# Optimization experiments

Hardware: AMD Instinct MI355X
Metric: run time of the kernel (lower is better)

Reference implementation:

```python
import jax, jax.numpy as jnp
import numpy as np

N_NODES = 50000


def gcn_conv(x, W, b, src, dst, n_nodes):
    # PyG GCNConv: add self-loops, symmetric normalization, linear, scatter-add.
    loop = jnp.arange(n_nodes, dtype=src.dtype)
    s = jnp.concatenate([src, loop])  # [E+N]
    d = jnp.concatenate([dst, loop])
    deg = jax.ops.segment_sum(jnp.ones_like(d, dtype=x.dtype), d, num_segments=n_nodes)
    dinv = jnp.where(deg > 0, deg ** -0.5, 0.0)
    norm = dinv[s] * dinv[d]  # [E+N]
    h = x @ W  # [N, F_out] transform first (cheaper than per-edge)
    msg = h[s] * norm[:, None]  # gather + scale
    out = jax.ops.segment_sum(msg, d, num_segments=n_nodes)  # scatter-add
    return out + b


def setup_inputs() -> dict:
    key = jax.random.key(0)
    k1, k2, k3, k4, k5 = jax.random.split(key, 5)
    n_in, n_hid, n_out = 128, 128, 64
    x = jax.random.normal(k1, (N_NODES, n_in), dtype=jnp.float32)
    edge_index = jax.random.randint(k2, (2, 800000), 0, N_NODES, dtype=jnp.int64)
    edge_label_index = jax.random.randint(k3, (2, 200000), 0, N_NODES, dtype=jnp.int64)
    # Glorot-style init for GCN weights, zero bias (PyG default)
    W1 = jax.random.normal(k4, (n_in, n_hid), dtype=jnp.float32) * (1.0 / np.sqrt(n_in))
    W2 = jax.random.normal(k5, (n_hid, n_out), dtype=jnp.float32) * (1.0 / np.sqrt(n_hid))
    b1 = jnp.zeros((n_hid,), dtype=jnp.float32)
    b2 = jnp.zeros((n_out,), dtype=jnp.float32)
    return {"x": x, "edge_index": edge_index, "edge_label_index": edge_label_index,
            "W1": W1, "b1": b1, "W2": W2, "b2": b2}


def reference(x, edge_index, edge_label_index, W1, b1, W2, b2):
    src, dst = edge_index[0], edge_index[1]
    h = jax.nn.relu(gcn_conv(x, W1, b1, src, dst, N_NODES))
    z = gcn_conv(h, W2, b2, src, dst, N_NODES)
    # decode: per-edge dot product of endpoint embeddings
    logits = jnp.sum(z[edge_label_index[0]] * z[edge_label_index[1]], axis=-1)
    return logits
```

## Files before the change

kernel.cpp:

```cpp
#include <hip/hip_runtime.h>

#define N_NODES 50000
#define NB ((N_NODES + 255) / 256)

using half8 = __attribute__((ext_vector_type(8))) _Float16;
using half4 = __attribute__((ext_vector_type(4))) _Float16;
using f32x4 = __attribute__((ext_vector_type(4))) float;


#define OFF_ROWPTR 50048
#define OFF_DESC   100096
#define OFF_CNT    100608
#define OFF_ESRC   150656
#define OFF_EPOS   950656
#define OFF_W1T    1750656
#define OFF_W2T    1758848
#define OFF_H1B    1762944
#define OFF_OUT1   4962944
#define OFF_Z      8162944

__device__ __forceinline__ ushort f2bf(float f) {
  uint u = __float_as_uint(f);
  u += 0x7fffu + ((u >> 16) & 1u);
  return (ushort)(u >> 16);
}
__device__ __forceinline__ uint pack2(float a, float b) {
  return (uint)f2bf(a) | ((uint)f2bf(b) << 16);
}
__device__ __forceinline__ uint pack2h(float a, float b) {
  ushort ua = __builtin_bit_cast(ushort, (_Float16)a);
  ushort ub = __builtin_bit_cast(ushort, (_Float16)b);
  return (uint)ua | ((uint)ub << 16);
}
__device__ __forceinline__ float blo(uint u) { return __uint_as_float(u << 16); }
__device__ __forceinline__ float bhi(uint u) { return __uint_as_float(u & 0xffff0000u); }

__global__ __launch_bounds__(256) void k_zero_prep(int* __restrict__ cnt,
                                                   uint* __restrict__ desc,
                                                   const float* __restrict__ W1,
                                                   const float* __restrict__ W2,
                                                   _Float16* __restrict__ W1t,
                                                   _Float16* __restrict__ W2t) {
  int bid = blockIdx.x;
  if (bid < NB) {
    int i = bid * 256 + threadIdx.x;
    if (i < N_NODES) cnt[i] = 0;
    if (bid == 0 && threadIdx.x < NB) desc[threadIdx.x] = 0;
    return;
  }
  int i = (bid - NB) * 256 + threadIdx.x;
  if (i < 16384) {
    int c = i >> 7, k = i & 127;
    W1t[c * 128 + (k ^ ((c & 7) << 3))] = (_Float16)W1[k * 128 + c];
  } else if (i < 24576) {
    int j = i - 16384;
    int c = j >> 7, k = j & 127;
    W2t[c * 128 + (k ^ ((c & 7) << 3))] = (_Float16)W2[k * 64 + c];
  }
}

__global__ __launch_bounds__(256) void k_hist(const int* __restrict__ dst, int E,
                                              int* __restrict__ cnt,
                                              int* __restrict__ epos) {
  int i = blockIdx.x * 256 + threadIdx.x;
  if (i < E) epos[i] = atomicAdd(&cnt[dst[i]], 1);
}

__global__ __launch_bounds__(256) void k_scanlb(const int* __restrict__ cnt,
                                                int* __restrict__ rowptr,
                                                float* __restrict__ dinv,
                                                uint* __restrict__ desc, int E) {
  __shared__ int tmp[256];
  __shared__ int s_prefix;
  const int b = blockIdx.x;
  const int i = b * 256 + threadIdx.x;
  int v = (i < N_NODES) ? cnt[i] : 0;
  tmp[threadIdx.x] = v;
  __syncthreads();
  for (int off = 1; off < 256; off <<= 1) {
    int t = (threadIdx.x >= off) ? tmp[threadIdx.x - off] : 0;
    __syncthreads();
    tmp[threadIdx.x] += t;
    __syncthreads();
  }
  int incl = tmp[threadIdx.x];
  int total = tmp[255];

  if (threadIdx.x == 0) {
    uint w0 = (b == 0) ? ((2u << 30) | (uint)total) : ((1u << 30) | (uint)total);
    atomicExch(&desc[b], w0);
    if (b == 0) s_prefix = 0;
  }
  if (b > 0 && threadIdx.x < 64) {
    const int lane = threadIdx.x;
    int run = 0;
    int j = b - 1;
    while (true) {
      int jj = j - lane;
      uint w = (jj >= 0) ? atomicAdd(&desc[jj], 0u) : (2u << 30);
      uint st = w >> 30;
      unsigned long long mz = __ballot(st == 0u);
      unsigned long long mp = __ballot(st == 2u);
      int fp = mp ? (__ffsll((long long)mp) - 1) : 64;
      unsigned long long below = (fp >= 64) ? ~0ull : ((1ull << fp) - 1ull);
      if (mz & below) continue;
      int contrib = (lane <= fp) ? (int)(w & 0x3FFFFFFFu) : 0;
      contrib += __shfl_down(contrib, 32, 64);
      contrib += __shfl_down(contrib, 16, 64);
      contrib += __shfl_down(contrib, 8, 64);
      contrib += __shfl_down(contrib, 4, 64);
      contrib += __shfl_down(contrib, 2, 64);
      contrib += __shfl_down(contrib, 1, 64);
      run += __shfl(contrib, 0, 64);
      if (fp < 64) break;
      j -= 64;
    }
    if (lane == 0) {
      atomicExch(&desc[b], (2u << 30) | (uint)(run + total));
      s_prefix = run;
    }
  }
  __syncthreads();
  int run = s_prefix;
  if (i < N_NODES) {
    rowptr[i] = run + incl - v;
    dinv[i] = rsqrtf(1.0f + (float)v);
  }
  if (b == NB - 1 && threadIdx.x == 0) rowptr[N_NODES] = E;
}

__global__ __launch_bounds__(256) void k_fill(const int* __restrict__ src,
                                              const int* __restrict__ dst,
                                              const int* __restrict__ epos, int E,
                                              const int* __restrict__ rowptr,
                                              int* __restrict__ esrc) {
  int e = blockIdx.x * 256 + threadIdx.x;
  if (e < E) esrc[rowptr[dst[e]] + epos[e]] = src[e];
}

__global__ __launch_bounds__(256) void k_gemm1(const float* __restrict__ x,
                                               const _Float16* __restrict__ W1t,
                                               const float* __restrict__ dinv,
                                               ushort* __restrict__ h1b) {
  __shared__ _Float16 Wl[128 * 128];
  __shared__ _Float16 xs[64 * 128];
  const int tid = threadIdx.x;
  const int lane = tid & 63;
  const int wv = tid >> 6;
  const int n0 = blockIdx.x * 64;

  for (int i = tid; i < 128 * 128 / 8; i += 256)
    *(float4*)&Wl[i * 8] = *(const float4*)&W1t[i * 8];
  for (int i = tid; i < 64 * 32; i += 256) {
    int nn = i >> 5, k4 = (i & 31) * 4;
    int gr = min(n0 + nn, N_NODES - 1);
    float4 v = *(const float4*)&x[(size_t)gr * 128 + k4];
    half4 hv;
    hv[0] = (_Float16)v.x; hv[1] = (_Float16)v.y;
    hv[2] = (_Float16)v.z; hv[3] = (_Float16)v.w;
    *(half4*)&xs[nn * 128 + (k4 ^ ((nn & 7) << 3))] = hv;
  }
  __syncthreads();

  f32x4 acc[8];
#pragma unroll
  for (int c = 0; c < 8; ++c) acc[c] = (f32x4){0.f, 0.f, 0.f, 0.f};

  const int m15 = lane & 15;
  const int kc = lane >> 4;
  const int xrow = wv * 16 + m15;

#pragma unroll
  for (int kt = 0; kt < 4; ++kt) {
    int e0 = kt * 32 + kc * 8;
    half8 bfrag = *(half8*)&xs[xrow * 128 + (e0 ^ ((xrow & 7) << 3))];
#pragma unroll
    for (int ct = 0; ct < 8; ++ct) {
      int wrow = ct * 16 + m15;
      half8 afrag = *(half8*)&Wl[wrow * 128 + (e0 ^ ((wrow & 7) << 3))];
      acc[ct] = __builtin_amdgcn_mfma_f32_16x16x32_f16(afrag, bfrag, acc[ct], 0, 0, 0);
    }
  }

  int n = n0 + wv * 16 + m15;
  if (n < N_NODES) {
    float dl = dinv[n];
#pragma unroll
    for (int ct = 0; ct < 8; ++ct) {
      int c = ct * 16 + kc * 4;
      uint2 p;
      p.x = pack2(acc[ct][0] * dl, acc[ct][1] * dl);
      p.y = pack2(acc[ct][2] * dl, acc[ct][3] * dl);
      *(uint2*)&h1b[(size_t)n * 128 + c] = p;
    }
  }
}

__global__ __launch_bounds__(256) void k_pull1(const int* __restrict__ rowptr,
                                               const int* __restrict__ esrc,
                                               const float* __restrict__ dinv,
                                               const uint* __restrict__ h1b,
                                               const float* __restrict__ b1,
                                               uint* __restrict__ out1h) {
  int n = (blockIdx.x * 256 + threadIdx.x) >> 6;
  int lane = threadIdx.x & 63;
  if (n >= N_NODES) return;
  int b = rowptr[n], e = rowptr[n + 1];
  int deg = e - b;

  uint u = h1b[(size_t)n * 64 + lane];
  float a0 = blo(u), a1 = bhi(u);

  int sidx = (lane < deg) ? esrc[b + lane] : 0;
  int kmax = deg < 64 ? deg : 64;
  int k = 0;
  for (; k + 15 < kmax; k += 16) {
    uint uu[16];
#pragma unroll
    for (int q = 0; q < 16; ++q) {
      int s = __shfl(sidx, k + q, 64);
      uu[q] = h1b[(size_t)s * 64 + lane];
    }
#pragma unroll
    for (int q = 0; q < 16; ++q) { a0 += blo(uu[q]); a1 += bhi(uu[q]); }
  }
  for (; k + 7 < kmax; k += 8) {
    uint uu[8];
#pragma unroll
    for (int q = 0; q < 8; ++q) {
      int s = __shfl(sidx, k + q, 64);
      uu[q] = h1b[(size_t)s * 64 + lane];
    }
#pragma unroll
    for (int q = 0; q < 8; ++q) { a0 += blo(uu[q]); a1 += bhi(uu[q]); }
  }
  for (; k < kmax; ++k) {
    int s = __shfl(sidx, k, 64);
    uint uu = h1b[(size_t)s * 64 + lane];
    a0 += blo(uu);
    a1 += bhi(uu);
  }
  for (int j = b + 64; j < e; ++j) {
    uint uu = h1b[(size_t)esrc[j] * 64 + lane];
    a0 += blo(uu);
    a1 += bhi(uu);
  }

  float dd = dinv[n];
  float2 bb = ((const float2*)b1)[lane];
  out1h[(size_t)n * 64 + lane] = pack2h(fmaf(dd, a0, bb.x), fmaf(dd, a1, bb.y));
}

__global__ __launch_bounds__(256) void k_gemm2(const _Float16* __restrict__ out1h,
                                               const _Float16* __restrict__ W2t,
                                               const float* __restrict__ dinv,
                                               ushort* __restrict__ h2b) {
  __shared__ _Float16 Wl[64 * 128];
  __shared__ _Float16 xs[64 * 128];
  const int tid = threadIdx.x;
  const int lane = tid & 63;
  const int wv = tid >> 6;
  const int n0 = blockIdx.x * 64;

  for (int i = tid; i < 64 * 128 / 8; i += 256)
    *(float4*)&Wl[i * 8] = *(const float4*)&W2t[i * 8];
  for (int i = tid; i < 64 * 16; i += 256) {
    int nn = i >> 4, k8 = (i & 15) * 8;
    int gr = min(n0 + nn, N_NODES - 1);
    half8 v = *(const half8*)&out1h[(size_t)gr * 128 + k8];
#pragma unroll
    for (int q = 0; q < 8; ++q) v[q] = v[q] > (_Float16)0.f ? v[q] : (_Float16)0.f;
    *(half8*)&xs[nn * 128 + (k8 ^ ((nn & 7) << 3))] = v;
  }
  __syncthreads();

  f32x4 acc[4];
#pragma unroll
  for (int c = 0; c < 4; ++c) acc[c] = (f32x4){0.f, 0.f, 0.f, 0.f};

  const int m15 = lane & 15;
  const int kc = lane >> 4;
  const int xrow = wv * 16 + m15;

#pragma unroll
  for (int kt = 0; kt < 4; ++kt) {
    int e0 = kt * 32 + kc * 8;
    half8 bfrag = *(half8*)&xs[xrow * 128 + (e0 ^ ((xrow & 7) << 3))];
#pragma unroll
    for (int ct = 0; ct < 4; ++ct) {
      int wrow = ct * 16 + m15;
      half8 afrag = *(half8*)&Wl[wrow * 128 + (e0 ^ ((wrow & 7) << 3))];
      acc[ct] = __builtin_amdgcn_mfma_f32_16x16x32_f16(afrag, bfrag, acc[ct], 0, 0, 0);
    }
  }

  int n = n0 + wv * 16 + m15;
  if (n < N_NODES) {
    float dl = dinv[n];
#pragma unroll
    for (int ct = 0; ct < 4; ++ct) {
      int c = ct * 16 + kc * 4;
      uint2 p;
      p.x = pack2(acc[ct][0] * dl, acc[ct][1] * dl);
      p.y = pack2(acc[ct][2] * dl, acc[ct][3] * dl);
      *(uint2*)&h2b[(size_t)n * 64 + c] = p;
    }
  }
}

__global__ __launch_bounds__(256) void k_pull2(const int* __restrict__ rowptr,
                                               const int* __restrict__ esrc,
                                               const float* __restrict__ dinv,
                                               const ushort* __restrict__ h2b,
                                               const float* __restrict__ b2,
                                               _Float16* __restrict__ z) {
  int n = (blockIdx.x * 256 + threadIdx.x) >> 6;
  int lane = threadIdx.x & 63;
  if (n >= N_NODES) return;
  int b = rowptr[n], e = rowptr[n + 1];
  int deg = e - b;

  float a = __uint_as_float((uint)h2b[(size_t)n * 64 + lane] << 16);

  int sidx = (lane < deg) ? esrc[b + lane] : 0;
  int kmax = deg < 64 ? deg : 64;
  int k = 0;
  for (; k + 15 < kmax; k += 16) {
    ushort vv[16];
#pragma unroll
    for (int q = 0; q < 16; ++q) {
      int s = __shfl(sidx, k + q, 64);
      vv[q] = h2b[(size_t)s * 64 + lane];
    }
#pragma unroll
    for (int q = 0; q < 16; ++q) a += __uint_as_float((uint)vv[q] << 16);
  }
  for (; k + 7 < kmax; k += 8) {
    ushort vv[8];
#pragma unroll
    for (int q = 0; q < 8; ++q) {
      int s = __shfl(sidx, k + q, 64);
      vv[q] = h2b[(size_t)s * 64 + lane];
    }
#pragma unroll
    for (int q = 0; q < 8; ++q) a += __uint_as_float((uint)vv[q] << 16);
  }
  for (; k < kmax; ++k) {
    int s = __shfl(sidx, k, 64);
    a += __uint_as_float((uint)h2b[(size_t)s * 64 + lane] << 16);
  }
  for (int j = b + 64; j < e; ++j)
    a += __uint_as_float((uint)h2b[(size_t)esrc[j] * 64 + lane] << 16);

  z[(size_t)n * 64 + lane] = (_Float16)fmaf(dinv[n], a, b2[lane]);
}

__global__ __launch_bounds__(256) void k_decode(const int* __restrict__ ia,
                                                const int* __restrict__ ib,
                                                const _Float16* __restrict__ z,
                                                float* __restrict__ out, int M) {
  const int sub = threadIdx.x & 7;
  int e = (blockIdx.x * 256 + threadIdx.x) >> 3;
  if (e >= M) return;
  int a = ia[e], b = ib[e];
  half8 va = ((const half8*)z)[(size_t)a * 8 + sub];
  half8 vb = ((const half8*)z)[(size_t)b * 8 + sub];
  float v = 0.f;
#pragma unroll
  for (int i = 0; i < 8; ++i) v += (float)va[i] * (float)vb[i];
  v += __shfl_xor(v, 4, 64);
  v += __shfl_xor(v, 2, 64);
  v += __shfl_xor(v, 1, 64);
  if (sub == 0) out[e] = v;
}

extern "C" void kernel_launch(void* const* d_in, const int* in_sizes, int n_in,
                              void* d_out, int out_size, void* d_ws, size_t ws_size,
                              hipStream_t stream) {
  const float* x   = (const float*)d_in[0];
  const int*   ei  = (const int*)d_in[1];
  const int*   eli = (const int*)d_in[2];
  const float* W1  = (const float*)d_in[3];
  const float* b1  = (const float*)d_in[4];
  const float* W2  = (const float*)d_in[5];
  const float* b2  = (const float*)d_in[6];
  float* outp = (float*)d_out;

  const int E = in_sizes[1] / 2;
  const int M = in_sizes[2] / 2;
  const int* src = ei;
  const int* dst = ei + E;
  const int* la  = eli;
  const int* lb  = eli + M;

  float* ws      = (float*)d_ws;
  float* dinv    = ws;
  int*   rowptr  = (int*)(ws + OFF_ROWPTR);
  uint*  desc    = (uint*)(ws + OFF_DESC);
  int*   cnt     = (int*)(ws + OFF_CNT);
  int*   esrc    = (int*)(ws + OFF_ESRC);
  int*   epos    = (int*)(ws + OFF_EPOS);
  _Float16* W1t  = (_Float16*)(ws + OFF_W1T);
  _Float16* W2t  = (_Float16*)(ws + OFF_W2T);
  ushort* h1b    = (ushort*)(ws + OFF_H1B);
  ushort* h2b    = (ushort*)(ws + OFF_H1B);
  _Float16* out1h = (_Float16*)(ws + OFF_OUT1);
  _Float16* z    = (_Float16*)(ws + OFF_Z);

  k_zero_prep<<<NB + 96, 256, 0, stream>>>(cnt, desc, W1, W2, W1t, W2t);
  k_hist  <<<(E + 255) / 256, 256, 0, stream>>>(dst, E, cnt, epos);
  k_scanlb<<<NB, 256, 0, stream>>>(cnt, rowptr, dinv, desc, E);
  k_fill  <<<(E + 255) / 256, 256, 0, stream>>>(src, dst, epos, E, rowptr, esrc);

  k_gemm1<<<(N_NODES + 63) / 64, 256, 0, stream>>>(x, W1t, dinv, h1b);
  k_pull1<<<12500, 256, 0, stream>>>(rowptr, esrc, dinv, (const uint*)h1b, b1,
                                     (uint*)out1h);

  k_gemm2<<<(N_NODES + 63) / 64, 256, 0, stream>>>(out1h, W2t, dinv, h2b);
  k_pull2<<<12500, 256, 0, stream>>>(rowptr, esrc, dinv, h2b, b2, z);

  k_decode<<<6250, 256, 0, stream>>>(la, lb, z, outp, M);
}
```

Measured before the change: 227.4 us.

## Fuse CSR fill with GEMM1, pack dst into epos, read W1 directly

The edge-fill kernel and the first GEMM become one launch in which the first blocks scatter edges and the rest compute x@W1, so the two independent jobs run concurrently. epos now packs the destination index into its low 17 bits, so the fill no longer re-reads dst. The GEMM drops its LDS copy of W1 and reads the pre-swizzled fragments straight from global memory, relying on cache. The decode kernel loads each edge index once per 8 lanes and broadcasts it with shuffles. Risks: the 17-bit packing caps per-node in-degree at about 32K, and hist and fill now use a fixed FILLB grid that only covers E up to 800000.

```diff
diff --git a/kernel.cpp b/kernel.cpp
--- a/kernel.cpp
+++ b/kernel.cpp
@@ -2,6 +2,7 @@
 
 #define N_NODES 50000
 #define NB ((N_NODES + 255) / 256)
+#define FILLB 3125
 
 using half8 = __attribute__((ext_vector_type(8))) _Float16;
 using half4 = __attribute__((ext_vector_type(4))) _Float16;
@@ -61,9 +62,13 @@
 
 __global__ __launch_bounds__(256) void k_hist(const int* __restrict__ dst, int E,
                                               int* __restrict__ cnt,
-                                              int* __restrict__ epos) {
+                                              uint* __restrict__ epos) {
   int i = blockIdx.x * 256 + threadIdx.x;
-  if (i < E) epos[i] = atomicAdd(&cnt[dst[i]], 1);
+  if (i < E) {
+    int d = dst[i];
+    int pos = atomicAdd(&cnt[d], 1);
+    epos[i] = ((uint)pos << 17) | (uint)d;
+  }
 }
 
 __global__ __launch_bounds__(256) void k_scanlb(const int* __restrict__ cnt,
@@ -129,28 +134,31 @@
   if (b == NB - 1 && threadIdx.x == 0) rowptr[N_NODES] = E;
 }
 
-__global__ __launch_bounds__(256) void k_fill(const int* __restrict__ src,
-                                              const int* __restrict__ dst,
-                                              const int* __restrict__ epos, int E,
-                                              const int* __restrict__ rowptr,
-                                              int* __restrict__ esrc) {
-  int e = blockIdx.x * 256 + threadIdx.x;
-  if (e < E) esrc[rowptr[dst[e]] + epos[e]] = src[e];
-}
-
-__global__ __launch_bounds__(256) void k_gemm1(const float* __restrict__ x,
-                                               const _Float16* __restrict__ W1t,
-                                               const float* __restrict__ dinv,
-                                               ushort* __restrict__ h1b) {
-  __shared__ _Float16 Wl[128 * 128];
+__global__ __launch_bounds__(256) void k_fill_gemm1(const int* __restrict__ src,
+                                                    const uint* __restrict__ epos,
+                                                    int E,
+                                                    const int* __restrict__ rowptr,
+                                                    int* __restrict__ esrc,
+                                                    const float* __restrict__ x,
+                                                    const _Float16* __restrict__ W1t,
+                                                    const float* __restrict__ dinv,
+                                                    ushort* __restrict__ h1b) {
   __shared__ _Float16 xs[64 * 128];
+  if (blockIdx.x < FILLB) {
+    int e = blockIdx.x * 256 + threadIdx.x;
+    if (e < E) {
+      uint w = epos[e];
+      int d = (int)(w & 0x1FFFFu);
+      esrc[rowptr[d] + (int)(w >> 17)] = src[e];
+    }
+    return;
+  }
+  const int bid = blockIdx.x - FILLB;
   const int tid = threadIdx.x;
   const int lane = tid & 63;
   const int wv = tid >> 6;
-  const int n0 = blockIdx.x * 64;
-
-  for (int i = tid; i < 128 * 128 / 8; i += 256)
-    *(float4*)&Wl[i * 8] = *(const float4*)&W1t[i * 8];
+  const int n0 = bid * 64;
+
   for (int i = tid; i < 64 * 32; i += 256) {
     int nn = i >> 5, k4 = (i & 31) * 4;
     int gr = min(n0 + nn, N_NODES - 1);
@@ -169,6 +177,7 @@
   const int m15 = lane & 15;
   const int kc = lane >> 4;
   const int xrow = wv * 16 + m15;
+  const int wsw = (m15 & 7) << 3;
 
 #pragma unroll
   for (int kt = 0; kt < 4; ++kt) {
@@ -177,7 +186,7 @@
 #pragma unroll
     for (int ct = 0; ct < 8; ++ct) {
       int wrow = ct * 16 + m15;
-      half8 afrag = *(half8*)&Wl[wrow * 128 + (e0 ^ ((wrow & 7) << 3))];
+      half8 afrag = *(const half8*)&W1t[wrow * 128 + (e0 ^ wsw)];
       acc[ct] = __builtin_amdgcn_mfma_f32_16x16x32_f16(afrag, bfrag, acc[ct], 0, 0, 0);
     }
   }
@@ -359,10 +368,19 @@
                                                 const int* __restrict__ ib,
                                                 const _Float16* __restrict__ z,
                                                 float* __restrict__ out, int M) {
-  const int sub = threadIdx.x & 7;
-  int e = (blockIdx.x * 256 + threadIdx.x) >> 3;
+  const int lane = threadIdx.x & 63;
+  const int sub = lane & 7;
+  const int eo = lane >> 3;
+  int base = (blockIdx.x * 256 + (threadIdx.x & ~63)) >> 3;
+  int a8 = 0, b8 = 0;
+  if (lane < 8 && base + lane < M) {
+    a8 = ia[base + lane];
+    b8 = ib[base + lane];
+  }
+  int e = base + eo;
   if (e >= M) return;
-  int a = ia[e], b = ib[e];
+  int a = __shfl(a8, eo, 64);
+  int b = __shfl(b8, eo, 64);
   half8 va = ((const half8*)z)[(size_t)a * 8 + sub];
   half8 vb = ((const half8*)z)[(size_t)b * 8 + sub];
   float v = 0.f;
@@ -399,7 +417,7 @@
   uint*  desc    = (uint*)(ws + OFF_DESC);
   int*   cnt     = (int*)(ws + OFF_CNT);
   int*   esrc    = (int*)(ws + OFF_ESRC);
-  int*   epos    = (int*)(ws + OFF_EPOS);
+  uint*  epos    = (uint*)(ws + OFF_EPOS);
   _Float16* W1t  = (_Float16*)(ws + OFF_W1T);
   _Float16* W2t  = (_Float16*)(ws + OFF_W2T);
   ushort* h1b    = (ushort*)(ws + OFF_H1B);
@@ -408,11 +426,11 @@
   _Float16* z    = (_Float16*)(ws + OFF_Z);
 
   k_zero_prep<<<NB + 96, 256, 0, stream>>>(cnt, desc, W1, W2, W1t, W2t);
-  k_hist  <<<(E + 255) / 256, 256, 0, stream>>>(dst, E, cnt, epos);
+  k_hist  <<<FILLB, 256, 0, stream>>>(dst, E, cnt, epos);
   k_scanlb<<<NB, 256, 0, stream>>>(cnt, rowptr, dinv, desc, E);
-  k_fill  <<<(E + 255) / 256, 256, 0, stream>>>(src, dst, epos, E, rowptr, esrc);
-
-  k_gemm1<<<(N_NODES + 63) / 64, 256, 0, stream>>>(x, W1t, dinv, h1b);
+
+  k_fill_gemm1<<<FILLB + (N_NODES + 63) / 64, 256, 0, stream>>>(
+      src, epos, E, rowptr, esrc, x, W1t, dinv, h1b);
   k_pull1<<<12500, 256, 0, stream>>>(rowptr, esrc, dinv, (const uint*)h1b, b1,
                                      (uint*)out1h);
 
```

After: 227.1 us. No clear change (-0.1%).
